# Performance work log

Hardware: AMD Instinct MI355X
Metric: run time of the kernel (lower is better)

Reference implementation:

```python
import jax, jax.numpy as jnp
import numpy as np

N_NODES = 50000
N_EDGES = 800000
F_IN = 512
HIDDEN = 128
N_CLASSES = 40


def setup_inputs() -> dict:
    key = jax.random.key(0)
    ks = jax.random.split(key, 5)
    x = jax.random.normal(ks[0], (N_NODES, F_IN), dtype=jnp.float32)
    edge_index = jax.random.randint(ks[1], (2, N_EDGES), 0, N_NODES, dtype=jnp.int32)
    # Glorot-ish init for GCNConv linear weights, zero bias (PyG default bias=True)
    W1 = jax.random.normal(ks[2], (F_IN, HIDDEN), dtype=jnp.float32) * (1.0 / np.sqrt(F_IN))
    b1 = jnp.zeros((HIDDEN,), dtype=jnp.float32)
    W2 = jax.random.normal(ks[3], (HIDDEN, N_CLASSES), dtype=jnp.float32) * (1.0 / np.sqrt(HIDDEN))
    b2 = jnp.zeros((N_CLASSES,), dtype=jnp.float32)
    return {"x": x, "edge_index": edge_index, "W1": W1, "b1": b1, "W2": W2, "b2": b2}


def _gcn_conv(x, W, b, row, col, n_nodes):
    """PyG GCNConv: linear transform, then symmetric-normalized aggregation.

    row/col already include self-loops. deg computed over col (in-degree),
    norm = d^{-1/2}[row] * d^{-1/2}[col], out[row] += norm * h[col].
    """
    h = x @ W  # [N, out]
    ones = jnp.ones(col.shape[0], dtype=h.dtype)
    deg = jax.ops.segment_sum(ones, col, num_segments=n_nodes)  # >=1 due to self-loops
    dinv = jax.lax.rsqrt(deg)
    norm = dinv[row] * dinv[col]  # [E]
    msgs = h[col] * norm[:, None]  # [E, out] gather + scale
    out = jax.ops.segment_sum(msgs, row, num_segments=n_nodes)  # scatter-add
    return out + b


def reference(x, edge_index, W1, b1, W2, b2):
    n = x.shape[0]
    loop = jnp.arange(n, dtype=edge_index.dtype)
    row = jnp.concatenate([edge_index[0], loop])
    col = jnp.concatenate([edge_index[1], loop])
    h = _gcn_conv(x, W1, b1, row, col, n)
    h = jax.nn.relu(h)
    # dropout with training=False is identity (eval-mode reference)
    out = _gcn_conv(h, W2, b2, row, col, n)
    return out
```

## Files before the change

kernel.cpp:

```cpp
#include <hip/hip_runtime.h>
#include <hip/hip_bf16.h>

#define N_NODES 50000
#define N_EDGES 800000
#define F_IN 512
#define HIDDEN 128
#define N_CLASSES 40
#define NSCAN 196

typedef __attribute__((ext_vector_type(4))) float f32x4;
typedef __attribute__((ext_vector_type(8))) short s16x8;

__device__ __forceinline__ unsigned bf16r(float f) {
    unsigned u = __float_as_uint(f);
    return (u + 0x7fffu + ((u >> 16) & 1u)) >> 16;
}
__device__ __forceinline__ unsigned pkbf(float lo, float hi) {
    return bf16r(lo) | (bf16r(hi) << 16);
}
__device__ __forceinline__ float bflo(unsigned u) { return __uint_as_float(u << 16); }
__device__ __forceinline__ float bfhi(unsigned u) { return __uint_as_float(u & 0xffff0000u); }

__global__ void init_kernel(int* __restrict__ rowcnt, int* __restrict__ colcnt,
                            int* __restrict__ cursor) {
    int i = blockIdx.x * 256 + threadIdx.x;
    if (i < N_NODES) { rowcnt[i] = 0; colcnt[i] = 0; cursor[i] = 0; }
}

__global__ void count_kernel(const int* __restrict__ row, const int* __restrict__ col,
                             int* __restrict__ rowcnt, int* __restrict__ colcnt) {
    int e = blockIdx.x * 256 + threadIdx.x;
    if (e < N_EDGES) {
        atomicAdd(&rowcnt[row[e]], 1);
        atomicAdd(&colcnt[col[e]], 1);
    }
}

__global__ void deg_fin_kernel(const int* __restrict__ colcnt, float* __restrict__ dinv) {
    int i = blockIdx.x * 256 + threadIdx.x;
    if (i < N_NODES) dinv[i] = rsqrtf(1.0f + (float)colcnt[i]);
}

__global__ void scan_blocks_kernel(const int* __restrict__ rowcnt, int* __restrict__ rowptr,
                                   int* __restrict__ partials) {
    __shared__ int s[256];
    const int tid = threadIdx.x;
    const int i = blockIdx.x * 256 + tid;
    const int v = (i < N_NODES) ? rowcnt[i] : 0;
    s[tid] = v;
    __syncthreads();
    #pragma unroll
    for (int off = 1; off < 256; off <<= 1) {
        int t = (tid >= off) ? s[tid - off] : 0;
        __syncthreads();
        s[tid] += t;
        __syncthreads();
    }
    if (i < N_NODES) rowptr[i] = s[tid] - v;
    if (tid == 255) partials[blockIdx.x] = s[255];
}

__global__ void scan_partials_kernel(int* __restrict__ partials) {
    __shared__ int s[256];
    const int tid = threadIdx.x;
    const int v = (tid < NSCAN) ? partials[tid] : 0;
    s[tid] = v;
    __syncthreads();
    #pragma unroll
    for (int off = 1; off < 256; off <<= 1) {
        int t = (tid >= off) ? s[tid - off] : 0;
        __syncthreads();
        s[tid] += t;
        __syncthreads();
    }
    if (tid < NSCAN) partials[tid] = s[tid] - v;
}

__global__ void scan_add_kernel(int* __restrict__ rowptr, const int* __restrict__ partials) {
    int i = blockIdx.x * 256 + threadIdx.x;
    if (i < N_NODES) rowptr[i] += partials[blockIdx.x];
    if (i == 0) rowptr[N_NODES] = N_EDGES;
}

__global__ void place_kernel(const int* __restrict__ row, const int* __restrict__ col,
                             const int* __restrict__ rowptr, int* __restrict__ cursor,
                             int* __restrict__ ecol) {
    int e = blockIdx.x * 256 + threadIdx.x;
    if (e < N_EDGES) {
        int r = row[e];
        int pos = rowptr[r] + atomicAdd(&cursor[r], 1);
        ecol[pos] = col[e];
    }
}

__global__ void w1frag_kernel(const float* __restrict__ W1, uint4* __restrict__ w1f) {
    int f = blockIdx.x * 256 + threadIdx.x;
    int lane = f & 63, u = (f >> 6) & 7, c = f >> 9;
    int k0 = c * 32 + ((lane >> 4) << 3), n = u * 16 + (lane & 15);
    float v[8];
    #pragma unroll
    for (int j = 0; j < 8; ++j) v[j] = W1[(size_t)(k0 + j) * HIDDEN + n];
    uint4 o;
    o.x = pkbf(v[0], v[1]); o.y = pkbf(v[2], v[3]);
    o.z = pkbf(v[4], v[5]); o.w = pkbf(v[6], v[7]);
    w1f[f] = o;
}

__global__ void w2frag_kernel(const float* __restrict__ W2, uint4* __restrict__ w2f) {
    int f = blockIdx.x * 256 + threadIdx.x;
    if (f >= 768) return;
    int lane = f & 63, u = (f >> 6) % 3, c = f / 192;
    int k0 = c * 32 + ((lane >> 4) << 3), n = u * 16 + (lane & 15);
    float v[8];
    #pragma unroll
    for (int j = 0; j < 8; ++j)
        v[j] = (n < N_CLASSES) ? W2[(size_t)(k0 + j) * N_CLASSES + n] : 0.0f;
    uint4 o;
    o.x = pkbf(v[0], v[1]); o.y = pkbf(v[2], v[3]);
    o.z = pkbf(v[4], v[5]); o.w = pkbf(v[6], v[7]);
    w2f[f] = o;
}

__global__ __launch_bounds__(256) void gemm1_kernel(
    const float* __restrict__ x, const uint4* __restrict__ w1f,
    const float* __restrict__ dinv, unsigned short* __restrict__ h1s)
{
    __shared__ uint4 XAf[256];
    const int tid  = threadIdx.x;
    const int wave = tid >> 6, lane = tid & 63;
    const int l16  = lane & 15, quad = lane >> 4;
    const int row0 = blockIdx.x * 64;

    f32x4 acc[4][2] = {};

    int sr = row0 + wave * 16 + l16;
    if (sr >= N_NODES) sr = N_NODES - 1;
    const float* xrow = x + (size_t)sr * F_IN + (quad << 3);

    for (int c = 0; c < F_IN / 32; ++c) {
        float4 a = *(const float4*)(xrow + c * 32);
        float4 b = *(const float4*)(xrow + c * 32 + 4);
        uint4 fr;
        fr.x = pkbf(a.x, a.y); fr.y = pkbf(a.z, a.w);
        fr.z = pkbf(b.x, b.y); fr.w = pkbf(b.z, b.w);
        XAf[tid] = fr;
        __syncthreads();

        uint4 t0 = w1f[(size_t)(c * 8 + wave * 2 + 0) * 64 + lane];
        uint4 t1 = w1f[(size_t)(c * 8 + wave * 2 + 1) * 64 + lane];
        s16x8 bf0 = *(s16x8*)&t0, bf1 = *(s16x8*)&t1;

        #pragma unroll
        for (int i = 0; i < 4; ++i) {
            uint4 ta = XAf[i * 64 + lane];
            s16x8 af = *(s16x8*)&ta;
            acc[i][0] = __builtin_amdgcn_mfma_f32_16x16x32_bf16(af, bf0, acc[i][0], 0, 0, 0);
            acc[i][1] = __builtin_amdgcn_mfma_f32_16x16x32_bf16(af, bf1, acc[i][1], 0, 0, 0);
        }
        __syncthreads();
    }

    const int n0 = wave * 32;
    #pragma unroll
    for (int i = 0; i < 4; ++i) {
        #pragma unroll
        for (int p = 0; p < 4; ++p) {
            int gr = row0 + i * 16 + quad * 4 + p;
            if (gr < N_NODES) {
                float s = dinv[gr];
                #pragma unroll
                for (int u = 0; u < 2; ++u)
                    h1s[(size_t)gr * HIDDEN + n0 + u * 16 + l16] =
                        (unsigned short)bf16r(acc[i][u][p] * s);
            }
        }
    }
}

__global__ __launch_bounds__(256) void gather1_kernel(
    const int* __restrict__ rowptr, const int* __restrict__ ecol,
    const float* __restrict__ dinv, const unsigned* __restrict__ h1u,
    const float* __restrict__ b1, unsigned* __restrict__ agg1u)
{
    const int wave = threadIdx.x >> 6, lane = threadIdx.x & 63;
    const int r = blockIdx.x * 4 + wave;
    if (r >= N_NODES) return;
    const int start = rowptr[r], end = rowptr[r + 1];

    float ax = 0.f, ay = 0.f, bx = 0.f, by = 0.f;
    float cx = 0.f, cy = 0.f, dx = 0.f, dy = 0.f;
    int e = start;
    for (; e + 3 < end; e += 4) {
        unsigned u0 = h1u[(size_t)ecol[e] * 64 + lane];
        unsigned u1 = h1u[(size_t)ecol[e + 1] * 64 + lane];
        unsigned u2 = h1u[(size_t)ecol[e + 2] * 64 + lane];
        unsigned u3 = h1u[(size_t)ecol[e + 3] * 64 + lane];
        ax += bflo(u0); ay += bfhi(u0); bx += bflo(u1); by += bfhi(u1);
        cx += bflo(u2); cy += bfhi(u2); dx += bflo(u3); dy += bfhi(u3);
    }
    for (; e < end; ++e) {
        unsigned u = h1u[(size_t)ecol[e] * 64 + lane];
        ax += bflo(u); ay += bfhi(u);
    }
    unsigned us = h1u[(size_t)r * 64 + lane];
    float sx = (ax + bx) + (cx + dx) + bflo(us);
    float sy = (ay + by) + (cy + dy) + bfhi(us);
    const float s = dinv[r];
    const float2 bb = *(const float2*)&b1[lane * 2];
    float ox = fmaxf(fmaf(s, sx, bb.x), 0.f);
    float oy = fmaxf(fmaf(s, sy, bb.y), 0.f);
    agg1u[(size_t)r * 64 + lane] = pkbf(ox, oy);
}

__global__ __launch_bounds__(256) void gemm2_kernel(
    const uint4* __restrict__ agg1q,
    const uint4* __restrict__ w2f,
    const float* __restrict__ dinv, float* __restrict__ h2s)
{
    __shared__ uint4 XAf[512];
    const int tid  = threadIdx.x;
    const int wave = tid >> 6, lane = tid & 63;
    const int l16  = lane & 15, quad = lane >> 4;
    const int row0 = blockIdx.x * 128;

    f32x4 acc[2][3] = {};

    int r1 = row0 + wave * 16 + l16;        if (r1 >= N_NODES) r1 = N_NODES - 1;
    int r2 = row0 + (4 + wave) * 16 + l16;  if (r2 >= N_NODES) r2 = N_NODES - 1;

    for (int c = 0; c < 4; ++c) {
        XAf[tid]       = agg1q[(size_t)r1 * 16 + c * 4 + quad];
        XAf[tid + 256] = agg1q[(size_t)r2 * 16 + c * 4 + quad];
        __syncthreads();

        s16x8 bf[3];
        #pragma unroll
        for (int u = 0; u < 3; ++u) {
            uint4 t = w2f[(size_t)(c * 3 + u) * 64 + lane];
            bf[u] = *(s16x8*)&t;
        }
        #pragma unroll
        for (int i = 0; i < 2; ++i) {
            uint4 ta = XAf[(wave * 2 + i) * 64 + lane];
            s16x8 af = *(s16x8*)&ta;
            #pragma unroll
            for (int u = 0; u < 3; ++u)
                acc[i][u] = __builtin_amdgcn_mfma_f32_16x16x32_bf16(af, bf[u], acc[i][u], 0, 0, 0);
        }
        __syncthreads();
    }

    #pragma unroll
    for (int i = 0; i < 2; ++i) {
        #pragma unroll
        for (int p = 0; p < 4; ++p) {
            int gr = row0 + (wave * 2 + i) * 16 + quad * 4 + p;
            if (gr < N_NODES) {
                float s = dinv[gr];
                #pragma unroll
                for (int u = 0; u < 3; ++u) {
                    int ncol = u * 16 + l16;
                    if (ncol < N_CLASSES)
                        h2s[(size_t)gr * N_CLASSES + ncol] = acc[i][u][p] * s;
                }
            }
        }
    }
}

__global__ __launch_bounds__(256) void gather2_kernel(
    const int* __restrict__ rowptr, const int* __restrict__ ecol,
    const float* __restrict__ dinv, const float* __restrict__ h2s,
    const float* __restrict__ b2, float* __restrict__ out)
{
    const int wave = threadIdx.x >> 6, lane = threadIdx.x & 63;
    const int r = blockIdx.x * 4 + wave;
    if (r >= N_NODES || lane >= N_CLASSES) return;
    const int start = rowptr[r], end = rowptr[r + 1];

    float a0 = 0.f, a1 = 0.f, a2 = 0.f, a3 = 0.f;
    int e = start;
    for (; e + 3 < end; e += 4) {
        a0 += h2s[(size_t)ecol[e] * N_CLASSES + lane];
        a1 += h2s[(size_t)ecol[e + 1] * N_CLASSES + lane];
        a2 += h2s[(size_t)ecol[e + 2] * N_CLASSES + lane];
        a3 += h2s[(size_t)ecol[e + 3] * N_CLASSES + lane];
    }
    for (; e < end; ++e) a0 += h2s[(size_t)ecol[e] * N_CLASSES + lane];
    float s = (a0 + a1) + (a2 + a3) + h2s[(size_t)r * N_CLASSES + lane];
    out[(size_t)r * N_CLASSES + lane] = fmaf(dinv[r], s, b2[lane]);
}

extern "C" void kernel_launch(void* const* d_in, const int* in_sizes, int n_in,
                              void* d_out, int out_size, void* d_ws, size_t ws_size,
                              hipStream_t stream)
{
    const float* x  = (const float*)d_in[0];
    const int*   ei = (const int*)d_in[1];
    const float* W1 = (const float*)d_in[2];
    const float* b1 = (const float*)d_in[3];
    const float* W2 = (const float*)d_in[4];
    const float* b2 = (const float*)d_in[5];
    const int* row = ei;
    const int* col = ei + N_EDGES;

    float* ws = (float*)d_ws;
    int*   rowcnt   = (int*)(ws);
    int*   colcnt   = (int*)(ws + 65536);
    int*   cursor   = (int*)(ws + 131072);
    float* dinv     = ws + 196608;
    int*   rowptr   = (int*)(ws + 262144);
    int*   partials = (int*)(ws + 327680);
    int*   ecol     = (int*)(ws + 335872);
    uint4* w1f      = (uint4*)(ws + 1155072);
    uint4* w2f      = (uint4*)(ws + 1187840);
    unsigned short* h1s = (unsigned short*)(ws + 1190912);
    unsigned*       h1u = (unsigned*)h1s;
    unsigned*  agg1u = (unsigned*)(ws + 4390912);
    uint4*     agg1q = (uint4*)agg1u;
    float*     h2s   = ws + 7590912;
    float*     out   = (float*)d_out;

    init_kernel<<<(N_NODES + 255) / 256, 256, 0, stream>>>(rowcnt, colcnt, cursor);
    count_kernel<<<(N_EDGES + 255) / 256, 256, 0, stream>>>(row, col, rowcnt, colcnt);
    deg_fin_kernel<<<(N_NODES + 255) / 256, 256, 0, stream>>>(colcnt, dinv);

    scan_blocks_kernel<<<NSCAN, 256, 0, stream>>>(rowcnt, rowptr, partials);
    scan_partials_kernel<<<1, 256, 0, stream>>>(partials);
    scan_add_kernel<<<NSCAN, 256, 0, stream>>>(rowptr, partials);
    place_kernel<<<(N_EDGES + 255) / 256, 256, 0, stream>>>(row, col, rowptr, cursor, ecol);

    w1frag_kernel<<<32, 256, 0, stream>>>(W1, w1f);
    w2frag_kernel<<<3, 256, 0, stream>>>(W2, w2f);

    gemm1_kernel<<<(N_NODES + 63) / 64, 256, 0, stream>>>(x, w1f, dinv, h1s);
    gather1_kernel<<<N_NODES / 4, 256, 0, stream>>>(rowptr, ecol, dinv, h1u, b1, agg1u);
    gemm2_kernel<<<(N_NODES + 127) / 128, 256, 0, stream>>>(agg1q, w2f, dinv, h2s);
    gather2_kernel<<<N_NODES / 4, 256, 0, stream>>>(rowptr, ecol, dinv, h2s, b2, out);
}
```

Measured before the change: 385.3 us.

## Overlap edge counting with GEMM1 in one launch and drop cursor atomics

Merges the edge-degree counting into the first GEMM launch by interleaving blocks, so the memory-bound atomic counting runs alongside the MFMA work. The dinv scaling of h1 moves out of the GEMM epilogue into the gather, which now loads dinv for each neighbour. The counting atomic's return value is saved as a per-edge slot, so the placement pass no longer needs a second atomic pass. The small weight-prep and init kernels are merged into one prep kernel plus a memset. The trade-offs are extra per-edge dinv gathers in the aggregation and an extra 800K-int buffer.

After: 329.7 us. 1.17x faster.

```diff
diff --git a/kernel.cpp b/kernel.cpp
--- a/kernel.cpp
+++ b/kernel.cpp
@@ -21,28 +21,107 @@
 __device__ __forceinline__ float bflo(unsigned u) { return __uint_as_float(u << 16); }
 __device__ __forceinline__ float bfhi(unsigned u) { return __uint_as_float(u & 0xffff0000u); }
 
-__global__ void init_kernel(int* __restrict__ rowcnt, int* __restrict__ colcnt,
-                            int* __restrict__ cursor) {
-    int i = blockIdx.x * 256 + threadIdx.x;
-    if (i < N_NODES) { rowcnt[i] = 0; colcnt[i] = 0; cursor[i] = 0; }
-}
-
-__global__ void count_kernel(const int* __restrict__ row, const int* __restrict__ col,
-                             int* __restrict__ rowcnt, int* __restrict__ colcnt) {
-    int e = blockIdx.x * 256 + threadIdx.x;
-    if (e < N_EDGES) {
-        atomicAdd(&rowcnt[row[e]], 1);
-        atomicAdd(&colcnt[col[e]], 1);
-    }
-}
-
-__global__ void deg_fin_kernel(const int* __restrict__ colcnt, float* __restrict__ dinv) {
-    int i = blockIdx.x * 256 + threadIdx.x;
-    if (i < N_NODES) dinv[i] = rsqrtf(1.0f + (float)colcnt[i]);
-}
-
-__global__ void scan_blocks_kernel(const int* __restrict__ rowcnt, int* __restrict__ rowptr,
-                                   int* __restrict__ partials) {
+__global__ void prep_kernel(const float* __restrict__ W1, const float* __restrict__ W2,
+                            uint4* __restrict__ w1f, uint4* __restrict__ w2f) {
+    int f = blockIdx.x * 256 + threadIdx.x;
+    if (f < 8192) {
+        int lane = f & 63, u = (f >> 6) & 7, c = f >> 9;
+        int k0 = c * 32 + ((lane >> 4) << 3), n = u * 16 + (lane & 15);
+        float v[8];
+        #pragma unroll
+        for (int j = 0; j < 8; ++j) v[j] = W1[(size_t)(k0 + j) * HIDDEN + n];
+        uint4 o;
+        o.x = pkbf(v[0], v[1]); o.y = pkbf(v[2], v[3]);
+        o.z = pkbf(v[4], v[5]); o.w = pkbf(v[6], v[7]);
+        w1f[f] = o;
+    } else if (f < 8960) {
+        int g = f - 8192;
+        int lane = g & 63, u = (g >> 6) % 3, c = g / 192;
+        int k0 = c * 32 + ((lane >> 4) << 3), n = u * 16 + (lane & 15);
+        float v[8];
+        #pragma unroll
+        for (int j = 0; j < 8; ++j)
+            v[j] = (n < N_CLASSES) ? W2[(size_t)(k0 + j) * N_CLASSES + n] : 0.0f;
+        uint4 o;
+        o.x = pkbf(v[0], v[1]); o.y = pkbf(v[2], v[3]);
+        o.z = pkbf(v[4], v[5]); o.w = pkbf(v[6], v[7]);
+        w2f[g] = o;
+    }
+}
+
+__global__ __launch_bounds__(256) void fused_kernel(
+    const float* __restrict__ x, const uint4* __restrict__ w1f,
+    unsigned short* __restrict__ h1s,
+    const int* __restrict__ row, const int* __restrict__ col,
+    int* __restrict__ rowcnt, int* __restrict__ colcnt, int* __restrict__ pos8)
+{
+    __shared__ uint4 XAf[256];
+    const int q = blockIdx.x / 5, rm = blockIdx.x % 5;
+
+    if (rm != 0) {
+        const int cb = q * 4 + rm - 1;
+        const int e = cb * 256 + threadIdx.x;
+        if (e < N_EDGES) {
+            pos8[e] = atomicAdd(&rowcnt[row[e]], 1);
+            atomicAdd(&colcnt[col[e]], 1);
+        }
+        return;
+    }
+
+    const int tid  = threadIdx.x;
+    const int wave = tid >> 6, lane = tid & 63;
+    const int l16  = lane & 15, quad = lane >> 4;
+    const int row0 = q * 64;
+
+    f32x4 acc[4][2] = {};
+
+    int sr = row0 + wave * 16 + l16;
+    if (sr >= N_NODES) sr = N_NODES - 1;
+    const float* xrow = x + (size_t)sr * F_IN + (quad << 3);
+
+    for (int c = 0; c < F_IN / 32; ++c) {
+        float4 a = *(const float4*)(xrow + c * 32);
+        float4 b = *(const float4*)(xrow + c * 32 + 4);
+        uint4 fr;
+        fr.x = pkbf(a.x, a.y); fr.y = pkbf(a.z, a.w);
+        fr.z = pkbf(b.x, b.y); fr.w = pkbf(b.z, b.w);
+        XAf[tid] = fr;
+        __syncthreads();
+
+        uint4 t0 = w1f[(size_t)(c * 8 + wave * 2 + 0) * 64 + lane];
+        uint4 t1 = w1f[(size_t)(c * 8 + wave * 2 + 1) * 64 + lane];
+        s16x8 bf0 = *(s16x8*)&t0, bf1 = *(s16x8*)&t1;
+
+        #pragma unroll
+        for (int i = 0; i < 4; ++i) {
+            uint4 ta = XAf[i * 64 + lane];
+            s16x8 af = *(s16x8*)&ta;
+            acc[i][0] = __builtin_amdgcn_mfma_f32_16x16x32_bf16(af, bf0, acc[i][0], 0, 0, 0);
+            acc[i][1] = __builtin_amdgcn_mfma_f32_16x16x32_bf16(af, bf1, acc[i][1], 0, 0, 0);
+        }
+        __syncthreads();
+    }
+
+    const int n0 = wave * 32;
+    #pragma unroll
+    for (int i = 0; i < 4; ++i) {
+        #pragma unroll
+        for (int p = 0; p < 4; ++p) {
+            int gr = row0 + i * 16 + quad * 4 + p;
+            if (gr < N_NODES) {
+                #pragma unroll
+                for (int u = 0; u < 2; ++u)
+                    h1s[(size_t)gr * HIDDEN + n0 + u * 16 + l16] =
+                        (unsigned short)bf16r(acc[i][u][p]);
+            }
+        }
+    }
+}
+
+__global__ void scan_blocks_kernel(const int* __restrict__ rowcnt,
+                                   const int* __restrict__ colcnt,
+                                   float* __restrict__ dinv,
+                                   int* __restrict__ rowptr, int* __restrict__ partials) {
     __shared__ int s[256];
     const int tid = threadIdx.x;
     const int i = blockIdx.x * 256 + tid;
@@ -56,7 +135,10 @@
         s[tid] += t;
         __syncthreads();
     }
-    if (i < N_NODES) rowptr[i] = s[tid] - v;
+    if (i < N_NODES) {
+        rowptr[i] = s[tid] - v;
+        dinv[i] = rsqrtf(1.0f + (float)colcnt[i]);
+    }
     if (tid == 255) partials[blockIdx.x] = s[255];
 }
 
@@ -83,98 +165,10 @@
 }
 
 __global__ void place_kernel(const int* __restrict__ row, const int* __restrict__ col,
-                             const int* __restrict__ rowptr, int* __restrict__ cursor,
+                             const int* __restrict__ rowptr, const int* __restrict__ pos8,
                              int* __restrict__ ecol) {
     int e = blockIdx.x * 256 + threadIdx.x;
-    if (e < N_EDGES) {
-        int r = row[e];
-        int pos = rowptr[r] + atomicAdd(&cursor[r], 1);
-        ecol[pos] = col[e];
-    }
-}
-
-__global__ void w1frag_kernel(const float* __restrict__ W1, uint4* __restrict__ w1f) {
-    int f = blockIdx.x * 256 + threadIdx.x;
-    int lane = f & 63, u = (f >> 6) & 7, c = f >> 9;
-    int k0 = c * 32 + ((lane >> 4) << 3), n = u * 16 + (lane & 15);
-    float v[8];
-    #pragma unroll
-    for (int j = 0; j < 8; ++j) v[j] = W1[(size_t)(k0 + j) * HIDDEN + n];
-    uint4 o;
-    o.x = pkbf(v[0], v[1]); o.y = pkbf(v[2], v[3]);
-    o.z = pkbf(v[4], v[5]); o.w = pkbf(v[6], v[7]);
-    w1f[f] = o;
-}
-
-__global__ void w2frag_kernel(const float* __restrict__ W2, uint4* __restrict__ w2f) {
-    int f = blockIdx.x * 256 + threadIdx.x;
-    if (f >= 768) return;
-    int lane = f & 63, u = (f >> 6) % 3, c = f / 192;
-    int k0 = c * 32 + ((lane >> 4) << 3), n = u * 16 + (lane & 15);
-    float v[8];
-    #pragma unroll
-    for (int j = 0; j < 8; ++j)
-        v[j] = (n < N_CLASSES) ? W2[(size_t)(k0 + j) * N_CLASSES + n] : 0.0f;
-    uint4 o;
-    o.x = pkbf(v[0], v[1]); o.y = pkbf(v[2], v[3]);
-    o.z = pkbf(v[4], v[5]); o.w = pkbf(v[6], v[7]);
-    w2f[f] = o;
-}
-
-__global__ __launch_bounds__(256) void gemm1_kernel(
-    const float* __restrict__ x, const uint4* __restrict__ w1f,
-    const float* __restrict__ dinv, unsigned short* __restrict__ h1s)
-{
-    __shared__ uint4 XAf[256];
-    const int tid  = threadIdx.x;
-    const int wave = tid >> 6, lane = tid & 63;
-    const int l16  = lane & 15, quad = lane >> 4;
-    const int row0 = blockIdx.x * 64;
-
-    f32x4 acc[4][2] = {};
-
-    int sr = row0 + wave * 16 + l16;
-    if (sr >= N_NODES) sr = N_NODES - 1;
-    const float* xrow = x + (size_t)sr * F_IN + (quad << 3);
-
-    for (int c = 0; c < F_IN / 32; ++c) {
-        float4 a = *(const float4*)(xrow + c * 32);
-        float4 b = *(const float4*)(xrow + c * 32 + 4);
-        uint4 fr;
-        fr.x = pkbf(a.x, a.y); fr.y = pkbf(a.z, a.w);
-        fr.z = pkbf(b.x, b.y); fr.w = pkbf(b.z, b.w);
-        XAf[tid] = fr;
-        __syncthreads();
-
-        uint4 t0 = w1f[(size_t)(c * 8 + wave * 2 + 0) * 64 + lane];
-        uint4 t1 = w1f[(size_t)(c * 8 + wave * 2 + 1) * 64 + lane];
-        s16x8 bf0 = *(s16x8*)&t0, bf1 = *(s16x8*)&t1;
-
-        #pragma unroll
-        for (int i = 0; i < 4; ++i) {
-            uint4 ta = XAf[i * 64 + lane];
-            s16x8 af = *(s16x8*)&ta;
-            acc[i][0] = __builtin_amdgcn_mfma_f32_16x16x32_bf16(af, bf0, acc[i][0], 0, 0, 0);
-            acc[i][1] = __builtin_amdgcn_mfma_f32_16x16x32_bf16(af, bf1, acc[i][1], 0, 0, 0);
-        }
-        __syncthreads();
-    }
-
-    const int n0 = wave * 32;
-    #pragma unroll
-    for (int i = 0; i < 4; ++i) {
-        #pragma unroll
-        for (int p = 0; p < 4; ++p) {
-            int gr = row0 + i * 16 + quad * 4 + p;
-            if (gr < N_NODES) {
-                float s = dinv[gr];
-                #pragma unroll
-                for (int u = 0; u < 2; ++u)
-                    h1s[(size_t)gr * HIDDEN + n0 + u * 16 + l16] =
-                        (unsigned short)bf16r(acc[i][u][p] * s);
-            }
-        }
-    }
+    if (e < N_EDGES) ecol[rowptr[row[e]] + pos8[e]] = col[e];
 }
 
 __global__ __launch_bounds__(256) void gather1_kernel(
@@ -191,21 +185,27 @@
     float cx = 0.f, cy = 0.f, dx = 0.f, dy = 0.f;
     int e = start;
     for (; e + 3 < end; e += 4) {
-        unsigned u0 = h1u[(size_t)ecol[e] * 64 + lane];
-        unsigned u1 = h1u[(size_t)ecol[e + 1] * 64 + lane];
-        unsigned u2 = h1u[(size_t)ecol[e + 2] * 64 + lane];
-        unsigned u3 = h1u[(size_t)ecol[e + 3] * 64 + lane];
-        ax += bflo(u0); ay += bfhi(u0); bx += bflo(u1); by += bfhi(u1);
-        cx += bflo(u2); cy += bfhi(u2); dx += bflo(u3); dy += bfhi(u3);
+        const int c0 = ecol[e], c1 = ecol[e + 1], c2 = ecol[e + 2], c3 = ecol[e + 3];
+        const float d0 = dinv[c0], d1 = dinv[c1], d2 = dinv[c2], d3 = dinv[c3];
+        unsigned u0 = h1u[(size_t)c0 * 64 + lane];
+        unsigned u1 = h1u[(size_t)c1 * 64 + lane];
+        unsigned u2 = h1u[(size_t)c2 * 64 + lane];
+        unsigned u3 = h1u[(size_t)c3 * 64 + lane];
+        ax = fmaf(bflo(u0), d0, ax); ay = fmaf(bfhi(u0), d0, ay);
+        bx = fmaf(bflo(u1), d1, bx); by = fmaf(bfhi(u1), d1, by);
+        cx = fmaf(bflo(u2), d2, cx); cy = fmaf(bfhi(u2), d2, cy);
+        dx = fmaf(bflo(u3), d3, dx); dy = fmaf(bfhi(u3), d3, dy);
     }
     for (; e < end; ++e) {
-        unsigned u = h1u[(size_t)ecol[e] * 64 + lane];
-        ax += bflo(u); ay += bfhi(u);
-    }
+        const int c = ecol[e];
+        const float d = dinv[c];
+        unsigned u = h1u[(size_t)c * 64 + lane];
+        ax = fmaf(bflo(u), d, ax); ay = fmaf(bfhi(u), d, ay);
+    }
+    const float s = dinv[r];
     unsigned us = h1u[(size_t)r * 64 + lane];
-    float sx = (ax + bx) + (cx + dx) + bflo(us);
-    float sy = (ay + by) + (cy + dy) + bfhi(us);
-    const float s = dinv[r];
+    float sx = (ax + bx) + (cx + dx) + bflo(us) * s;
+    float sy = (ay + by) + (cy + dy) + bfhi(us) * s;
     const float2 bb = *(const float2*)&b1[lane * 2];
     float ox = fmaxf(fmaf(s, sx, bb.x), 0.f);
     float oy = fmaxf(fmaf(s, sy, bb.y), 0.f);
@@ -213,8 +213,7 @@
 }
 
 __global__ __launch_bounds__(256) void gemm2_kernel(
-    const uint4* __restrict__ agg1q,
-    const uint4* __restrict__ w2f,
+    const uint4* __restrict__ agg1q, const uint4* __restrict__ w2f,
     const float* __restrict__ dinv, float* __restrict__ h2s)
 {
     __shared__ uint4 XAf[512];
@@ -307,33 +306,30 @@
     float* ws = (float*)d_ws;
     int*   rowcnt   = (int*)(ws);
     int*   colcnt   = (int*)(ws + 65536);
-    int*   cursor   = (int*)(ws + 131072);
-    float* dinv     = ws + 196608;
-    int*   rowptr   = (int*)(ws + 262144);
-    int*   partials = (int*)(ws + 327680);
-    int*   ecol     = (int*)(ws + 335872);
-    uint4* w1f      = (uint4*)(ws + 1155072);
-    uint4* w2f      = (uint4*)(ws + 1187840);
-    unsigned short* h1s = (unsigned short*)(ws + 1190912);
+    float* dinv     = ws + 131072;
+    int*   rowptr   = (int*)(ws + 196608);
+    int*   partials = (int*)(ws + 262144);
+    int*   pos8     = (int*)(ws + 270336);
+    int*   ecol     = (int*)(ws + 1089536);
+    uint4* w1f      = (uint4*)(ws + 1908736);
+    uint4* w2f      = (uint4*)(ws + 1941504);
+    unsigned short* h1s = (unsigned short*)(ws + 1944576);
     unsigned*       h1u = (unsigned*)h1s;
-    unsigned*  agg1u = (unsigned*)(ws + 4390912);
-    uint4*     agg1q = (uint4*)agg1u;
-    float*     h2s   = ws + 7590912;
-    float*     out   = (float*)d_out;
-
-    init_kernel<<<(N_NODES + 255) / 256, 256, 0, stream>>>(rowcnt, colcnt, cursor);
-    count_kernel<<<(N_EDGES + 255) / 256, 256, 0, stream>>>(row, col, rowcnt, colcnt);
-    deg_fin_kernel<<<(N_NODES + 255) / 256, 256, 0, stream>>>(colcnt, dinv);
-
-    scan_blocks_kernel<<<NSCAN, 256, 0, stream>>>(rowcnt, rowptr, partials);
+    unsigned* agg1u = (unsigned*)(ws + 5144576);
+    uint4*    agg1q = (uint4*)agg1u;
+    float*    h2s   = ws + 8344576;
+    float*    out   = (float*)d_out;
+
+    hipMemsetAsync(rowcnt, 0, 2 * 65536 * sizeof(int), stream);
+    prep_kernel<<<35, 256, 0, stream>>>(W1, W2, w1f, w2f);
+
+    fused_kernel<<<3910, 256, 0, stream>>>(x, w1f, h1s, row, col, rowcnt, colcnt, pos8);
+
+    scan_blocks_kernel<<<NSCAN, 256, 0, stream>>>(rowcnt, colcnt, dinv, rowptr, partials);
     scan_partials_kernel<<<1, 256, 0, stream>>>(partials);
     scan_add_kernel<<<NSCAN, 256, 0, stream>>>(rowptr, partials);
-    place_kernel<<<(N_EDGES + 255) / 256, 256, 0, stream>>>(row, col, rowptr, cursor, ecol);
-
-    w1frag_kernel<<<32, 256, 0, stream>>>(W1, w1f);
-    w2frag_kernel<<<3, 256, 0, stream>>>(W2, w2f);
-
-    gemm1_kernel<<<(N_NODES + 63) / 64, 256, 0, stream>>>(x, w1f, dinv, h1s);
+    place_kernel<<<3125, 256, 0, stream>>>(row, col, rowptr, pos8, ecol);
+
     gather1_kernel<<<N_NODES / 4, 256, 0, stream>>>(rowptr, ecol, dinv, h1u, b1, agg1u);
     gemm2_kernel<<<(N_NODES + 127) / 128, 256, 0, stream>>>(agg1q, w2f, dinv, h2s);
     gather2_kernel<<<N_NODES / 4, 256, 0, stream>>>(rowptr, ecol, dinv, h2s, b2, out);
```
